# Optimization experiments

Measured on AMD Instinct MI355X. Metric: run time of the kernel, lower is better.

## Reference

```python
import jax, jax.numpy as jnp
import numpy as np

N, E, D, C = 50000, 800000, 128, 7
BN_EPS = 1e-5


def _sage_conv(x, src, dst, Wl, Wr, b):
    # mean-aggregate neighbor messages per destination, then linear + root linear
    msgs = x[src]  # [E, D] irregular gather
    summed = jax.ops.segment_sum(msgs, dst, num_segments=N)
    cnt = jax.ops.segment_sum(jnp.ones((src.shape[0],), x.dtype), dst, num_segments=N)
    agg = summed / jnp.maximum(cnt, 1.0)[:, None]
    return agg @ Wl.T + x @ Wr.T + b


def _bn_eval(x, g, be):
    # running_mean=0, running_var=1 (eval mode)
    return x * (g / jnp.sqrt(1.0 + BN_EPS)) + be


def setup_inputs() -> dict:
    key = jax.random.key(0)
    ks = jax.random.split(key, 20)
    w = lambda k, s: jax.random.normal(k, s, dtype=jnp.float32) * 0.05
    inp = {
        "x": jax.random.normal(ks[0], (N, D), dtype=jnp.float32),
        "edge_index": jax.random.randint(ks[1], (2, E), 0, N, dtype=jnp.int64),
        "Wl0": w(ks[2], (D, D)), "Wr0": w(ks[3], (D, D)), "b0": jnp.zeros((D,), jnp.float32),
        "Wl1": w(ks[4], (D, D)), "Wr1": w(ks[5], (D, D)), "b1": jnp.zeros((D,), jnp.float32),
        "Wl2": w(ks[6], (D, D)), "Wr2": w(ks[7], (D, D)), "b2": jnp.zeros((D,), jnp.float32),
        "g0": jnp.ones((D,), jnp.float32), "be0": jnp.zeros((D,), jnp.float32),
        "g1": jnp.ones((D,), jnp.float32), "be1": jnp.zeros((D,), jnp.float32),
        "dW1": w(ks[8], (D, D)), "db1": jnp.zeros((D,), jnp.float32),
        "dW2": w(ks[9], (C, D)), "db2": jnp.zeros((C,), jnp.float32),
        "dW3": w(ks[10], (D, D)), "db3": jnp.zeros((D,), jnp.float32),
    }
    return inp


def reference(x, edge_index, Wl0, Wr0, b0, Wl1, Wr1, b1, Wl2, Wr2, b2,
              g0, be0, g1, be1, dW1, db1, dW2, db2, dW3, db3):
    src, dst = edge_index[0], edge_index[1]
    h = _sage_conv(x, src, dst, Wl0, Wr0, b0)
    h = jax.nn.relu(_bn_eval(h, g0, be0))  # dropout is identity in eval
    h = _sage_conv(h, src, dst, Wl1, Wr1, b1)
    h = jax.nn.relu(_bn_eval(h, g1, be1))
    h = _sage_conv(h, src, dst, Wl2, Wr2, b2)
    recon_x1 = h @ dW1.T + db1
    recon_x2 = h @ dW2.T + db2
    recon_x3 = h @ dW3.T + db3
    return (recon_x1, recon_x2, recon_x3)
```

## Files before the change

kernel.cpp:

```cpp
#include <hip/hip_runtime.h>
#include <hip/hip_fp16.h>

static constexpr float kBnEps = 1e-5f;
static constexpr int MAXB = 1024;

typedef __attribute__((ext_vector_type(8))) _Float16 f16x8;
typedef __attribute__((ext_vector_type(4))) float f32x4;

__global__ void detect_k(const int* __restrict__ eb, int* __restrict__ flag) {
    int l = threadIdx.x;
    int v = eb[2 * l + 1];
    unsigned long long m = __ballot(v == 0);
    if (l == 0) flag[0] = (m == ~0ull) ? 1 : 0;
}

__device__ __forceinline__ int edge_src(const int* eb, int is64, int E, int e) {
    return is64 ? eb[2 * e] : eb[e];
}
__device__ __forceinline__ int edge_dst(const int* eb, int is64, int E, int e) {
    return is64 ? eb[2 * E + 2 * e] : eb[E + e];
}

__global__ __launch_bounds__(256) void histA_k(const int* __restrict__ eb,
                                               const int* __restrict__ flag,
                                               int* __restrict__ gcnt, int E,
                                               int nbuck) {
    __shared__ int lh[MAXB];
    for (int i = threadIdx.x; i < nbuck; i += 256) lh[i] = 0;
    __syncthreads();
    int is64 = flag[0];
    int base = blockIdx.x * 4096;
#pragma unroll
    for (int i = 0; i < 16; ++i) {
        int e = base + i * 256 + threadIdx.x;
        if (e < E) {
            int d = edge_dst(eb, is64, E, e);
            atomicAdd(&lh[d >> 7], 1);
        }
    }
    __syncthreads();
    for (int i = threadIdx.x; i < nbuck; i += 256) {
        int c = lh[i];
        if (c) atomicAdd(&gcnt[i], c);
    }
}

__global__ __launch_bounds__(512) void scanB_k(const int* __restrict__ gcnt,
                                               int* __restrict__ gbase,
                                               int* __restrict__ gcur,
                                               int* __restrict__ offs, int E,
                                               int n, int nbuck) {
    __shared__ int s[512];
    int tid = threadIdx.x;
    int v = (tid < nbuck) ? gcnt[tid] : 0;
    s[tid] = v;
    __syncthreads();
    for (int d = 1; d < 512; d <<= 1) {
        int t = (tid >= d) ? s[tid - d] : 0;
        __syncthreads();
        s[tid] += t;
        __syncthreads();
    }
    if (tid < nbuck) {
        gbase[tid] = s[tid] - v;
        gcur[tid] = s[tid] - v;
    }
    if (tid == 0) {
        gbase[nbuck] = E;
        offs[n] = E;
    }
}

__global__ __launch_bounds__(256) void binC_k(const int* __restrict__ eb,
                                              const int* __restrict__ flag,
                                              int* __restrict__ gcur,
                                              unsigned* __restrict__ bins, int E,
                                              int nbuck) {
    __shared__ int lh[MAXB];
    __shared__ int lcur[MAXB];
    for (int i = threadIdx.x; i < nbuck; i += 256) lh[i] = 0;
    __syncthreads();
    int is64 = flag[0];
    int base = blockIdx.x * 4096;
    int ds[16], ss[16];
#pragma unroll
    for (int i = 0; i < 16; ++i) {
        int e = base + i * 256 + threadIdx.x;
        ds[i] = -1;
        if (e < E) {
            ds[i] = edge_dst(eb, is64, E, e);
            ss[i] = edge_src(eb, is64, E, e);
            atomicAdd(&lh[ds[i] >> 7], 1);
        }
    }
    __syncthreads();
    for (int b = threadIdx.x; b < nbuck; b += 256) {
        int c = lh[b];
        lcur[b] = c ? atomicAdd(&gcur[b], c) : 0;
    }
    __syncthreads();
#pragma unroll
    for (int i = 0; i < 16; ++i) {
        if (ds[i] >= 0) {
            int bkt = ds[i] >> 7;
            int p = atomicAdd(&lcur[bkt], 1);
            bins[p] = ((unsigned)ss[i] << 7) | (unsigned)(ds[i] & 127);
        }
    }
}

__global__ __launch_bounds__(256) void csrD_k(const unsigned* __restrict__ bins,
                                              const int* __restrict__ gbase,
                                              int* __restrict__ offs,
                                              int* __restrict__ csr, int n) {
    int b = blockIdx.x;
    __shared__ int hist[128];
    __shared__ int s[128];
    __shared__ int cur[128];
    int tid = threadIdx.x;
    if (tid < 128) hist[tid] = 0;
    __syncthreads();
    int base = gbase[b], endb = gbase[b + 1], m = endb - base;
    for (int i = tid; i < m; i += 256) atomicAdd(&hist[bins[base + i] & 127u], 1);
    __syncthreads();
    int v = 0;
    if (tid < 128) {
        v = hist[tid];
        s[tid] = v;
    }
    __syncthreads();
    for (int d = 1; d < 128; d <<= 1) {
        int t = (tid >= d && tid < 128) ? s[tid - d] : 0;
        __syncthreads();
        if (tid < 128) s[tid] += t;
        __syncthreads();
    }
    if (tid < 128) {
        int excl = s[tid] - v;
        int dst = b * 128 + tid;
        if (dst < n) offs[dst] = base + excl;
        cur[tid] = base + excl;
    }
    __syncthreads();
    for (int i = tid; i < m; i += 256) {
        unsigned u = bins[base + i];
        int p = atomicAdd(&cur[u & 127u], 1);
        csr[p] = (int)(u >> 7);
    }
}

__global__ void cvtx_k(const float* __restrict__ in, __half* __restrict__ out, int total8) {
    int i = blockIdx.x * blockDim.x + threadIdx.x;
    if (i >= total8) return;
    float4 v0 = ((const float4*)in)[2 * i];
    float4 v1 = ((const float4*)in)[2 * i + 1];
    __half2 h0 = __floats2half2_rn(v0.x, v0.y);
    __half2 h1 = __floats2half2_rn(v0.z, v0.w);
    __half2 h2 = __floats2half2_rn(v1.x, v1.y);
    __half2 h3 = __floats2half2_rn(v1.z, v1.w);
    uint4 o;
    o.x = *(uint*)&h0; o.y = *(uint*)&h1; o.z = *(uint*)&h2; o.w = *(uint*)&h3;
    ((uint4*)out)[i] = o;
}

__global__ void cvtw_k(const float* __restrict__ Wl0, const float* __restrict__ Wr0,
                       const float* __restrict__ Wl1, const float* __restrict__ Wr1,
                       const float* __restrict__ Wl2, const float* __restrict__ Wr2,
                       const float* __restrict__ dW1, const float* __restrict__ dW3,
                       const float* __restrict__ dW2,
                       __half* __restrict__ Wcat, __half* __restrict__ dWcat) {
    int idx = blockIdx.x * 256 + threadIdx.x;
    if (idx < 3 * 32768) {
        int l = idx >> 15;
        int rem = idx & 32767;
        int nn = rem >> 8;
        int k = rem & 255;
        const float* Wl = (l == 0) ? Wl0 : (l == 1) ? Wl1 : Wl2;
        const float* Wr = (l == 0) ? Wr0 : (l == 1) ? Wr1 : Wr2;
        float v = (k < 128) ? Wl[nn * 128 + k] : Wr[nn * 128 + (k - 128)];
        Wcat[idx] = __float2half_rn(v);
    } else if (idx < 3 * 32768 + 3 * 16384) {
        int j = idx - 3 * 32768;
        int blk = j >> 14;
        int r = (j & 16383) >> 7;
        int c = j & 127;
        float v;
        if (blk == 0) v = dW1[r * 128 + c];
        else if (blk == 1) v = dW3[r * 128 + c];
        else v = (r < 7) ? dW2[r * 128 + c] : 0.f;
        dWcat[j] = __float2half_rn(v);
    }
}

__global__ __launch_bounds__(256) void agg_k(const __half* __restrict__ Xh,
                                             const int* __restrict__ offs,
                                             const int* __restrict__ csr,
                                             __half* __restrict__ aggh, int n) {
    int gt = blockIdx.x * blockDim.x + threadIdx.x;
    int node = gt >> 6;
    int lane = threadIdx.x & 63;
    int grp = lane >> 4;
    int lg = lane & 15;
    if (node >= n) return;
    int beg = offs[node], end = offs[node + 1];
    int len = end - beg;
    const f16x8* Xp = (const f16x8*)Xh;
    float acc[8];
#pragma unroll
    for (int k = 0; k < 8; ++k) acc[k] = 0.f;
    for (int j0 = 0; j0 < len; j0 += 32) {
        int jj[8];
        bool ok[8];
        f16x8 v[8];
#pragma unroll
        for (int t = 0; t < 8; ++t) {
            int j = j0 + grp * 8 + t;
            ok[t] = j < len;
            jj[t] = csr[beg + (ok[t] ? j : 0)];
        }
#pragma unroll
        for (int t = 0; t < 8; ++t)
            if (ok[t]) v[t] = Xp[(size_t)jj[t] * 16 + lg];
#pragma unroll
        for (int t = 0; t < 8; ++t)
            if (ok[t]) {
#pragma unroll
                for (int k = 0; k < 8; ++k) acc[k] += (float)v[t][k];
            }
    }
#pragma unroll
    for (int k = 0; k < 8; ++k) {
        acc[k] += __shfl_xor(acc[k], 16, 64);
        acc[k] += __shfl_xor(acc[k], 32, 64);
    }
    if (grp == 0) {
        float inv = 1.0f / fmaxf((float)len, 1.0f);
        f16x8 o;
#pragma unroll
        for (int k = 0; k < 8; ++k) o[k] = (_Float16)(acc[k] * inv);
        ((f16x8*)aggh)[(size_t)node * 16 + lg] = o;
    }
}

template <int KTOT, bool TWO_SRC, bool BN_RELU, bool OUT16, bool HEADS>
__global__ __launch_bounds__(256) void mgemm_k(
    const __half* __restrict__ A0, const __half* __restrict__ A1,
    const __half* __restrict__ Bw, const float* __restrict__ bias,
    const float* __restrict__ g, const float* __restrict__ be,
    void* __restrict__ outv, const float* __restrict__ bias2,
    void* __restrict__ outv2, const float* __restrict__ bias3,
    void* __restrict__ outv3, int n) {
    constexpr int ROWB = KTOT * 2 + 16;
    __shared__ char sA[128 * ROWB];

    int ncol = 128, ostride = 128;
    if (HEADS) {
        int y = blockIdx.y;
        Bw += (size_t)y * 128 * KTOT;
        if (y == 1) { bias = bias2; outv = outv2; }
        if (y == 2) { bias = bias3; outv = outv3; ncol = 7; ostride = 7; }
    }

    const int tid = threadIdx.x;
    const int lane = tid & 63;
    const int wid = tid >> 6;
    const int wm = wid & 1;
    const int wn = wid >> 1;
    const int row0 = blockIdx.x * 128;

    constexpr int CPR = KTOT / 8;
#pragma unroll
    for (int i = 0; i < (128 * CPR) / 256; ++i) {
        int idx = tid + i * 256;
        int r = idx / CPR;
        int c = idx % CPR;
        int rg = row0 + r;
        float4 v = make_float4(0.f, 0.f, 0.f, 0.f);
        if (rg < n) {
            if (TWO_SRC)
                v = (c < 16) ? *(const float4*)(A0 + (size_t)rg * 128 + c * 8)
                             : *(const float4*)(A1 + (size_t)rg * 128 + (c - 16) * 8);
            else
                v = *(const float4*)(A0 + (size_t)rg * 128 + c * 8);
        }
        *(float4*)(&sA[r * ROWB + c * 16]) = v;
    }

    f32x4 acc[4][4];
#pragma unroll
    for (int mi = 0; mi < 4; ++mi)
#pragma unroll
        for (int ni = 0; ni < 4; ++ni) acc[mi][ni] = (f32x4){0.f, 0.f, 0.f, 0.f};

    __syncthreads();

    const int bcol = wn * 64;
    constexpr int KH = KTOT / 128;
#pragma unroll
    for (int kh = 0; kh < KH; ++kh) {
        f16x8 bfr[4][4];
#pragma unroll
        for (int ni = 0; ni < 4; ++ni)
#pragma unroll
            for (int kt = 0; kt < 4; ++kt) {
                int col = bcol + ni * 16 + (lane & 15);
                int ko = kh * 128 + kt * 32 + (lane >> 4) * 8;
                bfr[ni][kt] = *(const f16x8*)(Bw + (size_t)col * KTOT + ko);
            }
#pragma unroll
        for (int mi = 0; mi < 4; ++mi) {
            int rl = wm * 64 + mi * 16 + (lane & 15);
            const char* base = &sA[rl * ROWB + kh * 256 + (lane >> 4) * 16];
            f16x8 afr[4];
#pragma unroll
            for (int kt = 0; kt < 4; ++kt) afr[kt] = *(const f16x8*)(base + kt * 64);
#pragma unroll
            for (int kt = 0; kt < 4; ++kt)
#pragma unroll
                for (int ni = 0; ni < 4; ++ni)
                    acc[mi][ni] = __builtin_amdgcn_mfma_f32_16x16x32_f16(
                        afr[kt], bfr[ni][kt], acc[mi][ni], 0, 0, 0);
        }
    }

#pragma unroll
    for (int ni = 0; ni < 4; ++ni) {
        int col = bcol + ni * 16 + (lane & 15);
        if (HEADS && col >= ncol) continue;
        float bv = bias[col];
        float gs = 0.f, bes = 0.f;
        if (BN_RELU) {
            gs = g[col] / sqrtf(1.0f + kBnEps);
            bes = be[col];
        }
#pragma unroll
        for (int mi = 0; mi < 4; ++mi) {
#pragma unroll
            for (int r = 0; r < 4; ++r) {
                int row = row0 + wm * 64 + mi * 16 + (lane >> 4) * 4 + r;
                if (row < n) {
                    float v = acc[mi][ni][r] + bv;
                    if (BN_RELU) v = fmaxf(v * gs + bes, 0.f);
                    if (OUT16)
                        ((__half*)outv)[(size_t)row * 128 + col] = __float2half_rn(v);
                    else
                        ((float*)outv)[(size_t)row * ostride + col] = v;
                }
            }
        }
    }
}

extern "C" void kernel_launch(void* const* d_in, const int* in_sizes, int n_in,
                              void* d_out, int out_size, void* d_ws, size_t ws_size,
                              hipStream_t stream) {
    const float* x   = (const float*)d_in[0];
    const int*   eb  = (const int*)d_in[1];
    const float* Wl0 = (const float*)d_in[2];
    const float* Wr0 = (const float*)d_in[3];
    const float* b0  = (const float*)d_in[4];
    const float* Wl1 = (const float*)d_in[5];
    const float* Wr1 = (const float*)d_in[6];
    const float* b1  = (const float*)d_in[7];
    const float* Wl2 = (const float*)d_in[8];
    const float* Wr2 = (const float*)d_in[9];
    const float* b2  = (const float*)d_in[10];
    const float* g0  = (const float*)d_in[11];
    const float* be0 = (const float*)d_in[12];
    const float* g1  = (const float*)d_in[13];
    const float* be1 = (const float*)d_in[14];
    const float* dW1 = (const float*)d_in[15];
    const float* db1 = (const float*)d_in[16];
    const float* dW2 = (const float*)d_in[17];
    const float* db2 = (const float*)d_in[18];
    const float* dW3 = (const float*)d_in[19];
    const float* db3 = (const float*)d_in[20];

    const int n = in_sizes[0] / 128;
    const int E = in_sizes[1] / 2;
    const int nbuck = (n + 127) >> 7;

    char* ws = (char*)d_ws;
    size_t off = 0;
    auto alloc = [&](size_t bytes) -> void* {
        void* p = ws + off;
        off = (off + bytes + 255) & ~(size_t)255;
        return p;
    };
    int*      flag  = (int*)alloc(16);
    int*      gcnt  = (int*)alloc(MAXB * 4);
    int*      gbase = (int*)alloc((MAXB + 1) * 4);
    int*      gcur  = (int*)alloc(MAXB * 4);
    unsigned* bins  = (unsigned*)alloc((size_t)E * 4);
    int*      csr   = (int*)alloc((size_t)E * 4);
    int*      offs  = (int*)alloc((size_t)(n + 1) * 4);
    __half*   x_h   = (__half*)alloc((size_t)n * 128 * 2);
    __half*   agg_h = (__half*)alloc((size_t)n * 128 * 2);
    __half*   h0    = (__half*)alloc((size_t)n * 128 * 2);
    __half*   h1    = (__half*)alloc((size_t)n * 128 * 2);
    __half*   h2    = h0;
    __half*   Wcat  = (__half*)alloc(3 * 32768 * 2);
    __half*   dWcat = (__half*)alloc(3 * 16384 * 2);

    float* out0 = (float*)d_out;
    float* out1 = out0 + (size_t)n * 128;
    float* out2 = out1 + (size_t)n * 7;

    hipMemsetAsync(gcnt, 0, MAXB * 4, stream);

    const int ggrid = (n + 127) / 128;
    const int agg_grid = (n * 64 + 255) / 256;
    const int chunk_grid = (E + 4095) / 4096;

    detect_k<<<1, 64, 0, stream>>>(eb, flag);
    histA_k<<<chunk_grid, 256, 0, stream>>>(eb, flag, gcnt, E, nbuck);
    scanB_k<<<1, 512, 0, stream>>>(gcnt, gbase, gcur, offs, E, n, nbuck);
    binC_k<<<chunk_grid, 256, 0, stream>>>(eb, flag, gcur, bins, E, nbuck);
    csrD_k<<<nbuck, 256, 0, stream>>>(bins, gbase, offs, csr, n);

    cvtx_k<<<(n * 16 + 255) / 256, 256, 0, stream>>>(x, x_h, n * 16);
    cvtw_k<<<(147456 + 255) / 256, 256, 0, stream>>>(Wl0, Wr0, Wl1, Wr1, Wl2, Wr2,
                                                     dW1, dW3, dW2, Wcat, dWcat);

    agg_k<<<agg_grid, 256, 0, stream>>>(x_h, offs, csr, agg_h, n);
    mgemm_k<256, true, true, true, false><<<ggrid, 256, 0, stream>>>(
        agg_h, x_h, Wcat, b0, g0, be0, h0, nullptr, nullptr, nullptr, nullptr, n);
    agg_k<<<agg_grid, 256, 0, stream>>>(h0, offs, csr, agg_h, n);
    mgemm_k<256, true, true, true, false><<<ggrid, 256, 0, stream>>>(
        agg_h, h0, Wcat + 32768, b1, g1, be1, h1, nullptr, nullptr, nullptr, nullptr, n);
    agg_k<<<agg_grid, 256, 0, stream>>>(h1, offs, csr, agg_h, n);
    mgemm_k<256, true, false, true, false><<<ggrid, 256, 0, stream>>>(
        agg_h, h1, Wcat + 65536, b2, nullptr, nullptr, h2, nullptr, nullptr, nullptr,
        nullptr, n);
    mgemm_k<128, false, false, false, true><<<dim3(ggrid, 3), 256, 0, stream>>>(
        h2, nullptr, dWcat, db1, nullptr, nullptr, out0, db3, out2, db2, out1, n);
}
```

Measured before the change: 265.5 us.

## Fuse neighbor mean-aggregation into the SAGE GEMM kernel's shared-memory load

Removes the separate aggregation kernel and computes each tile's mean-aggregated neighbor rows directly inside the GEMM block, writing them into shared memory beside the root features. This drops the agg_h intermediate's global write and read and two kernel launches per layer. In exchange, each wave now walks 32 destination nodes serially, gathering one 4-byte half2 per lane per neighbor, so there is less memory-level parallelism than the old 16-byte-per-lane gather. Only about 391 blocks run with the gather inside the GEMM, so occupancy and latency hiding may suffer.

```diff
diff --git a/kernel.cpp b/kernel.cpp
--- a/kernel.cpp
+++ b/kernel.cpp
@@ -192,59 +192,10 @@
     }
 }
 
-__global__ __launch_bounds__(256) void agg_k(const __half* __restrict__ Xh,
-                                             const int* __restrict__ offs,
-                                             const int* __restrict__ csr,
-                                             __half* __restrict__ aggh, int n) {
-    int gt = blockIdx.x * blockDim.x + threadIdx.x;
-    int node = gt >> 6;
-    int lane = threadIdx.x & 63;
-    int grp = lane >> 4;
-    int lg = lane & 15;
-    if (node >= n) return;
-    int beg = offs[node], end = offs[node + 1];
-    int len = end - beg;
-    const f16x8* Xp = (const f16x8*)Xh;
-    float acc[8];
-#pragma unroll
-    for (int k = 0; k < 8; ++k) acc[k] = 0.f;
-    for (int j0 = 0; j0 < len; j0 += 32) {
-        int jj[8];
-        bool ok[8];
-        f16x8 v[8];
-#pragma unroll
-        for (int t = 0; t < 8; ++t) {
-            int j = j0 + grp * 8 + t;
-            ok[t] = j < len;
-            jj[t] = csr[beg + (ok[t] ? j : 0)];
-        }
-#pragma unroll
-        for (int t = 0; t < 8; ++t)
-            if (ok[t]) v[t] = Xp[(size_t)jj[t] * 16 + lg];
-#pragma unroll
-        for (int t = 0; t < 8; ++t)
-            if (ok[t]) {
-#pragma unroll
-                for (int k = 0; k < 8; ++k) acc[k] += (float)v[t][k];
-            }
-    }
-#pragma unroll
-    for (int k = 0; k < 8; ++k) {
-        acc[k] += __shfl_xor(acc[k], 16, 64);
-        acc[k] += __shfl_xor(acc[k], 32, 64);
-    }
-    if (grp == 0) {
-        float inv = 1.0f / fmaxf((float)len, 1.0f);
-        f16x8 o;
-#pragma unroll
-        for (int k = 0; k < 8; ++k) o[k] = (_Float16)(acc[k] * inv);
-        ((f16x8*)aggh)[(size_t)node * 16 + lg] = o;
-    }
-}
-
-template <int KTOT, bool TWO_SRC, bool BN_RELU, bool OUT16, bool HEADS>
+template <int KTOT, bool GATHER, bool BN_RELU, bool OUT16, bool HEADS>
 __global__ __launch_bounds__(256) void mgemm_k(
-    const __half* __restrict__ A0, const __half* __restrict__ A1,
+    const __half* __restrict__ src, const int* __restrict__ offs,
+    const int* __restrict__ csr,
     const __half* __restrict__ Bw, const float* __restrict__ bias,
     const float* __restrict__ g, const float* __restrict__ be,
     void* __restrict__ outv, const float* __restrict__ bias2,
@@ -268,22 +219,65 @@
     const int wn = wid >> 1;
     const int row0 = blockIdx.x * 128;
 
-    constexpr int CPR = KTOT / 8;
-#pragma unroll
-    for (int i = 0; i < (128 * CPR) / 256; ++i) {
-        int idx = tid + i * 256;
-        int r = idx / CPR;
-        int c = idx % CPR;
-        int rg = row0 + r;
-        float4 v = make_float4(0.f, 0.f, 0.f, 0.f);
-        if (rg < n) {
-            if (TWO_SRC)
-                v = (c < 16) ? *(const float4*)(A0 + (size_t)rg * 128 + c * 8)
-                             : *(const float4*)(A1 + (size_t)rg * 128 + (c - 16) * 8);
-            else
-                v = *(const float4*)(A0 + (size_t)rg * 128 + c * 8);
-        }
-        *(float4*)(&sA[r * ROWB + c * 16]) = v;
+    if (GATHER) {
+#pragma unroll
+        for (int i = 0; i < 8; ++i) {
+            int idx = tid + i * 256;
+            int r = idx >> 4;
+            int c = (idx & 15);
+            int rg = row0 + r;
+            float4 v = make_float4(0.f, 0.f, 0.f, 0.f);
+            if (rg < n) v = *(const float4*)(src + (size_t)rg * 128 + c * 8);
+            *(float4*)(&sA[r * ROWB + (c + 16) * 16]) = v;
+        }
+        const uint* Xp = (const uint*)src;
+#pragma unroll 1
+        for (int d = 0; d < 32; ++d) {
+            int dstLocal = wid * 32 + d;
+            int node = row0 + dstLocal;
+            float a0 = 0.f, a1 = 0.f;
+            int len = 0;
+            if (node < n) {
+                int beg = offs[node];
+                len = offs[node + 1] - beg;
+                for (int j0 = 0; j0 < len; j0 += 16) {
+                    int idxv[16];
+                    float wv[16];
+#pragma unroll
+                    for (int t = 0; t < 16; ++t) {
+                        int jj = j0 + t;
+                        bool ok = jj < len;
+                        idxv[t] = csr[beg + (ok ? jj : 0)];
+                        wv[t] = ok ? 1.f : 0.f;
+                    }
+                    uint v[16];
+#pragma unroll
+                    for (int t = 0; t < 16; ++t)
+                        v[t] = Xp[(size_t)idxv[t] * 64 + lane];
+#pragma unroll
+                    for (int t = 0; t < 16; ++t) {
+                        __half2 h = *(__half2*)&v[t];
+                        a0 += wv[t] * __low2float(h);
+                        a1 += wv[t] * __high2float(h);
+                    }
+                }
+            }
+            float inv = 1.0f / fmaxf((float)len, 1.0f);
+            __half2 o = __floats2half2_rn(a0 * inv, a1 * inv);
+            *(__half2*)(&sA[dstLocal * ROWB + lane * 4]) = o;
+        }
+    } else {
+        constexpr int CPR = KTOT / 8;
+#pragma unroll
+        for (int i = 0; i < (128 * CPR) / 256; ++i) {
+            int idx = tid + i * 256;
+            int r = idx / CPR;
+            int c = idx % CPR;
+            int rg = row0 + r;
+            float4 v = make_float4(0.f, 0.f, 0.f, 0.f);
+            if (rg < n) v = *(const float4*)(src + (size_t)rg * 128 + c * 8);
+            *(float4*)(&sA[r * ROWB + c * 16]) = v;
+        }
     }
 
     f32x4 acc[4][4];
@@ -395,7 +389,6 @@
     int*      csr   = (int*)alloc((size_t)E * 4);
     int*      offs  = (int*)alloc((size_t)(n + 1) * 4);
     __half*   x_h   = (__half*)alloc((size_t)n * 128 * 2);
-    __half*   agg_h = (__half*)alloc((size_t)n * 128 * 2);
     __half*   h0    = (__half*)alloc((size_t)n * 128 * 2);
     __half*   h1    = (__half*)alloc((size_t)n * 128 * 2);
     __half*   h2    = h0;
@@ -409,7 +402,6 @@
     hipMemsetAsync(gcnt, 0, MAXB * 4, stream);
 
     const int ggrid = (n + 127) / 128;
-    const int agg_grid = (n * 64 + 255) / 256;
     const int chunk_grid = (E + 4095) / 4096;
 
     detect_k<<<1, 64, 0, stream>>>(eb, flag);
@@ -422,16 +414,15 @@
     cvtw_k<<<(147456 + 255) / 256, 256, 0, stream>>>(Wl0, Wr0, Wl1, Wr1, Wl2, Wr2,
                                                      dW1, dW3, dW2, Wcat, dWcat);
 
-    agg_k<<<agg_grid, 256, 0, stream>>>(x_h, offs, csr, agg_h, n);
     mgemm_k<256, true, true, true, false><<<ggrid, 256, 0, stream>>>(
-        agg_h, x_h, Wcat, b0, g0, be0, h0, nullptr, nullptr, nullptr, nullptr, n);
-    agg_k<<<agg_grid, 256, 0, stream>>>(h0, offs, csr, agg_h, n);
+        x_h, offs, csr, Wcat, b0, g0, be0, h0, nullptr, nullptr, nullptr, nullptr, n);
     mgemm_k<256, true, true, true, false><<<ggrid, 256, 0, stream>>>(
-        agg_h, h0, Wcat + 32768, b1, g1, be1, h1, nullptr, nullptr, nullptr, nullptr, n);
-    agg_k<<<agg_grid, 256, 0, stream>>>(h1, offs, csr, agg_h, n);
+        h0, offs, csr, Wcat + 32768, b1, g1, be1, h1, nullptr, nullptr, nullptr,
+        nullptr, n);
     mgemm_k<256, true, false, true, false><<<ggrid, 256, 0, stream>>>(
-        agg_h, h1, Wcat + 65536, b2, nullptr, nullptr, h2, nullptr, nullptr, nullptr,
-        nullptr, n);
+        h1, offs, csr, Wcat + 65536, b2, nullptr, nullptr, h2, nullptr, nullptr,
+        nullptr, nullptr, n);
     mgemm_k<128, false, false, false, true><<<dim3(ggrid, 3), 256, 0, stream>>>(
-        h2, nullptr, dWcat, db1, nullptr, nullptr, out0, db3, out2, db2, out1, n);
-}
+        h2, nullptr, nullptr, dWcat, db1, nullptr, nullptr, out0, db3, out2, db2,
+        out1, n);
+}
```

Result: slower. 351.2 us (+32.3%).
